# Performance work log

Hardware: AMD Instinct MI355X
Metric: run time of the kernel (lower is better)

Reference implementation:

```python
import jax, jax.numpy as jnp
import numpy as np

D = 1024
H = 16
HD = D // H
EPS = 1e-5

def _layernorm(x, g, b):
    mu = jnp.mean(x, axis=-1, keepdims=True)
    var = jnp.mean(jnp.square(x - mu), axis=-1, keepdims=True)
    return (x - mu) * jax.lax.rsqrt(var + EPS) * g + b

def setup_inputs() -> dict:
    key = jax.random.key(0)
    ks = jax.random.split(key, 12)
    B, Sq, Skv = 8, 1024, 1024
    s = 1.0 / np.sqrt(D)  # xavier-ish scale
    return {
        "Q": jax.random.normal(ks[0], (B, Sq, D), jnp.float32),
        "K": jax.random.normal(ks[1], (B, Skv, D), jnp.float32),
        "key_padding_mask": jnp.ones((B, Skv), jnp.int32),
        "Wq": jax.random.normal(ks[2], (D, D), jnp.float32) * s,
        "bq": jnp.zeros((D,), jnp.float32),
        "Wk": jax.random.normal(ks[3], (D, D), jnp.float32) * s,
        "bk": jnp.zeros((D,), jnp.float32),
        "Wv": jax.random.normal(ks[4], (D, D), jnp.float32) * s,
        "bv": jnp.zeros((D,), jnp.float32),
        "Wp": jax.random.normal(ks[5], (D, D), jnp.float32) * s,
        "bp": jnp.zeros((D,), jnp.float32),
        "g0": jnp.ones((D,), jnp.float32),
        "beta0": jnp.zeros((D,), jnp.float32),
        "g1": jnp.ones((D,), jnp.float32),
        "beta1": jnp.zeros((D,), jnp.float32),
    }

def reference(Q, K, key_padding_mask, Wq, bq, Wk, bk, Wv, bv, Wp, bp, g0, beta0, g1, beta1):
    B, Sq, _ = Q.shape
    q = Q @ Wq + bq                      # [B,Sq,D]
    k = K @ Wk + bk                      # [B,Skv,D]
    v = K @ Wv + bv
    qh = q.reshape(B, Sq, H, HD).transpose(0, 2, 1, 3)   # [B,H,Sq,hd]
    kh = k.reshape(B, -1, H, HD).transpose(0, 2, 1, 3)   # [B,H,Skv,hd]
    vh = v.reshape(B, -1, H, HD).transpose(0, 2, 1, 3)
    attn = jnp.einsum('bhqd,bhkd->bhqk', qh, kh) / np.sqrt(HD)
    pad = (key_padding_mask == 0)[:, None, None, :]      # [B,1,1,Skv]
    attn = jnp.where(pad, -jnp.inf, attn)
    attn = jax.nn.softmax(attn, axis=-1)
    ctx = jnp.einsum('bhqk,bhkd->bhqd', attn, vh)        # [B,H,Sq,hd]
    ctx = ctx.transpose(0, 2, 1, 3).reshape(B, Sq, H * HD)
    o = _layernorm(q + ctx, g0, beta0)
    o = _layernorm(o + jax.nn.gelu(o @ Wp + bp, approximate=False), g1, beta1)
    return o
```

## Files before the change

kernel.cpp:

```cpp
#include <hip/hip_runtime.h>
#include <hip/hip_bf16.h>
#include <math.h>

#define DEV __device__ __forceinline__

typedef __bf16 bf16;
typedef __bf16 bf16x8 __attribute__((ext_vector_type(8)));
typedef __bf16 bf16x4 __attribute__((ext_vector_type(4)));
typedef __bf16 bf16x2 __attribute__((ext_vector_type(2)));
typedef float f32x4 __attribute__((ext_vector_type(4)));
typedef float f32x16 __attribute__((ext_vector_type(16)));
typedef int i32x2 __attribute__((ext_vector_type(2)));
typedef unsigned int u32;
typedef unsigned long long u64;

static constexpr int BATCH = 8, S = 1024, D = 1024, H = 16, HD = 64;
static constexpr int M = BATCH * S;

static constexpr float QSCALE = 0.18033688f;
static constexpr float INVQSCALE = 5.54517744f;

DEV f32x4 mfma16(bf16x8 a, bf16x8 b, f32x4 c) {
  return __builtin_amdgcn_mfma_f32_16x16x32_bf16(a, b, c, 0, 0, 0);
}
DEV f32x16 mfma32(bf16x8 a, bf16x8 b, f32x16 c) {
  return __builtin_amdgcn_mfma_f32_32x32x16_bf16(a, b, c, 0, 0, 0);
}

DEV void gload_lds16(const void* g, void* l) {
  __builtin_amdgcn_global_load_lds(
      (__attribute__((address_space(1))) void*)(g),
      (__attribute__((address_space(3))) void*)(l), 16, 0, 0);
}

DEV bf16x8 lds_read8(const void* base, int byteoff) {
  return *(const bf16x8*)((const char*)base + byteoff);
}

DEV u32 packbf(float a, float b) {
  bf16x2 t = { (bf16)a, (bf16)b };
  return __builtin_bit_cast(u32, t);
}


__global__ void cvt_bf16_kernel(const float* __restrict__ in0, bf16* __restrict__ out0,
                                const float* __restrict__ in1, bf16* __restrict__ out1, int n) {
  const float* in = blockIdx.y ? in1 : in0;
  bf16* out = blockIdx.y ? out1 : out0;
  int i = (blockIdx.x * blockDim.x + threadIdx.x) * 4;
  int stride = gridDim.x * blockDim.x * 4;
  for (; i < n; i += stride) {
    float4 v = *(const float4*)(in + i);
    bf16x4 o = { (bf16)v.x, (bf16)v.y, (bf16)v.z, (bf16)v.w };
    *(bf16x4*)(out + i) = o;
  }
}

__global__ void transpose_cvt_kernel(const float* __restrict__ w0, bf16* __restrict__ o0,
                                     const float* __restrict__ w1, bf16* __restrict__ o1,
                                     const float* __restrict__ w2, bf16* __restrict__ o2,
                                     const float* __restrict__ w3, bf16* __restrict__ o3) {
  const int z = blockIdx.z;
  const float* in = z == 0 ? w0 : z == 1 ? w1 : z == 2 ? w2 : w3;
  bf16* out = z == 0 ? o0 : z == 1 ? o1 : z == 2 ? o2 : o3;
  __shared__ float t[32][33];
  int n0 = blockIdx.x * 32, k0 = blockIdx.y * 32;
  int tx = threadIdx.x, ty = threadIdx.y;
  for (int i = 0; i < 32; i += 8)
    t[ty + i][tx] = in[(size_t)(k0 + ty + i) * D + n0 + tx];
  __syncthreads();
  for (int i = 0; i < 32; i += 8)
    out[(size_t)(n0 + ty + i) * D + k0 + tx] = (bf16)t[tx][ty + i];
}


DEV void gemm_body(const bf16* A, const bf16* Bt, const float* bias,
                   bf16* Cb, float osc, bf16* As, bf16* Bs) {
  constexpr int K = 1024, N = 1024, BK = 32;
  const int tid = threadIdx.x, lane = tid & 63, wave = tid >> 6;
  const int lo = lane & 15, g = lane >> 4;
  int f = blockIdx.y * 8 + blockIdx.x;
  f = (f & 7) * 64 + (f >> 3);
  const int bm = f >> 3, bn = f & 7;
  const int wr = wave >> 1, wc = wave & 1;
  f32x4 acc[4][4] = {};
  const char* Ab = (const char*)(A + (size_t)bm * 128 * K);
  const char* Bb = (const char*)(Bt + (size_t)bn * 128 * K);

  const int srow[2] = { (wave * 2 + 0) * 16 + (lane >> 2), (wave * 2 + 1) * 16 + (lane >> 2) };
  const int sslot = lane & 3;

  for (int kt = 0; kt < K / BK; ++kt) {
    __syncthreads();
    const int k0b = kt * (BK * 2);
    for (int i = 0; i < 2; ++i) {
      int cbase = (wave * 2 + i) * 1024;
      int row = srow[i];
      int scol = ((sslot ^ (row & 3)) << 4);
      gload_lds16(Ab + (size_t)row * (K * 2) + k0b + scol, (char*)As + cbase);
      gload_lds16(Bb + (size_t)row * (K * 2) + k0b + scol, (char*)Bs + cbase);
    }
    __syncthreads();
    bf16x8 af[4], bfr[4];
    for (int mi = 0; mi < 4; ++mi) {
      int ar = wr * 64 + mi * 16 + lo;
      af[mi] = lds_read8(As, ar * 64 + ((g ^ (ar & 3)) << 4));
    }
    for (int ni = 0; ni < 4; ++ni) {
      int br = wc * 64 + ni * 16 + lo;
      bfr[ni] = lds_read8(Bs, br * 64 + ((g ^ (br & 3)) << 4));
    }
    for (int mi = 0; mi < 4; ++mi)
      for (int ni = 0; ni < 4; ++ni)
        acc[mi][ni] = mfma16(af[mi], bfr[ni], acc[mi][ni]);
  }

  const int rbase = bm * 128 + wr * 64;
  const int cbase = bn * 128 + wc * 64;
  for (int ni = 0; ni < 4; ++ni) {
    int col = cbase + ni * 16 + lo;
    float bv = bias[col];
    for (int mi = 0; mi < 4; ++mi) {
      int row0 = rbase + mi * 16 + g * 4;
      for (int r = 0; r < 4; ++r) {
        float v = acc[mi][ni][r] + bv;
        Cb[(size_t)(row0 + r) * N + col] = (bf16)(v * osc);
      }
    }
  }
}

__global__ __launch_bounds__(256) void gemm_qkv_kernel(
    const bf16* __restrict__ Qb, const bf16* __restrict__ Kb,
    const bf16* __restrict__ Wqt, const bf16* __restrict__ Wkt, const bf16* __restrict__ Wvt,
    const float* __restrict__ bq, const float* __restrict__ bk, const float* __restrict__ bv,
    bf16* __restrict__ qb, bf16* __restrict__ kb, bf16* __restrict__ vb)
{
  __shared__ bf16 As[128 * 32];
  __shared__ bf16 Bs[128 * 32];
  const int z = blockIdx.z;
  if (z == 0)      gemm_body(Qb, Wqt, bq, qb, QSCALE, As, Bs);
  else if (z == 1) gemm_body(Kb, Wkt, bk, kb, 1.f, As, Bs);
  else             gemm_body(Kb, Wvt, bv, vb, 1.f, As, Bs);
}

__global__ __launch_bounds__(256) void gemm_p_kernel(
    const bf16* __restrict__ A, const bf16* __restrict__ Bt,
    const float* __restrict__ bias, bf16* __restrict__ Cb)
{
  __shared__ bf16 As[128 * 32];
  __shared__ bf16 Bs[128 * 32];
  gemm_body(A, Bt, bias, Cb, 1.f, As, Bs);
}


DEV int swz(int row, int colb) { return row * 128 + (colb ^ ((row & 7) << 4)); }

__global__ __launch_bounds__(256, 3) void attn_kernel(
    const bf16* __restrict__ q, const bf16* __restrict__ k, const bf16* __restrict__ v,
    const int* __restrict__ mask, float* __restrict__ ctx)
{
  __shared__ bf16 Kl[2][64 * 64];
  __shared__ bf16 Vt[2][64 * 64];
  const int tid = threadIdx.x, lane = tid & 63, wave = tid >> 6;
  const int hi = lane >> 5, lq = lane & 31;
  const int wg = blockIdx.x;
  const int xcd = wg & 7, ix = wg >> 3;
  const int bh = xcd * 16 + (ix & 15);
  const int qt = ix >> 4;
  const int b = bh >> 4, h = bh & 15;
  const int q0 = qt * 128 + wave * 32;
  const size_t base = (size_t)b * S * D + (size_t)h * HD;

  bf16x8 qf[4];
#pragma unroll
  for (int hc = 0; hc < 4; ++hc)
    qf[hc] = *(const bf16x8*)(q + base + (size_t)(q0 + lq) * D + hc * 16 + hi * 8);

  f32x16 oaccT[2] = {};
  float mrow = -3e38f, lrow = 0.f;

  bf16x8 kst[2], vst[2];
  const int koff = tid * 16;
  const int krow = koff >> 7, kcol = koff & 127;

#define LOADK(KV0)                                                              \
  {                                                                             \
    _Pragma("unroll")                                                           \
    for (int rr = 0; rr < 2; ++rr)                                              \
      kst[rr] = *(const bf16x8*)((const char*)(k + base +                       \
                 (size_t)((KV0) + rr * 32 + krow) * D) + kcol);                 \
    _Pragma("unroll")                                                           \
    for (int rr = 0; rr < 2; ++rr) {                                            \
      int kvr = rr * 32 + wave * 8;                                             \
      _Pragma("unroll")                                                         \
      for (int i = 0; i < 8; ++i)                                               \
        vst[rr][i] = v[base + (size_t)((KV0) + kvr + i) * D + lane];            \
    }                                                                           \
  }

#define WRITEK(BI)                                                              \
  {                                                                             \
    _Pragma("unroll")                                                           \
    for (int rr = 0; rr < 2; ++rr)                                              \
      *(bf16x8*)((char*)Kl[BI] + swz(rr * 32 + krow, kcol)) = kst[rr];          \
    _Pragma("unroll")                                                           \
    for (int rr = 0; rr < 2; ++rr)                                              \
      *(bf16x8*)((char*)Vt[BI] + swz(lane, (rr * 32 + wave * 8) * 2)) = vst[rr];\
  }

  LOADK(0);
  WRITEK(0);

  for (int kt = 0; kt < S / 64; ++kt) {
    const int cur = kt & 1;
    const int kv0 = kt * 64;
    __syncthreads();
    if (kt < S / 64 - 1) LOADK(kv0 + 64);

    const char* Kb_ = (const char*)Kl[cur];
    const char* Vb_ = (const char*)Vt[cur];

    u64 mv = __ballot(mask[b * S + kv0 + lane] != 0);

    f32x16 sacc[2];
    __builtin_amdgcn_s_setprio(1);
#pragma unroll
    for (int sub = 0; sub < 2; ++sub) {
      f32x16 a = {};
#pragma unroll
      for (int hc = 0; hc < 4; ++hc) {
        bf16x8 kf = lds_read8(Kb_, swz(sub * 32 + lq, hc * 32 + hi * 16));
        a = mfma32(kf, qf[hc], a);
      }
      sacc[sub] = a;
    }
    __builtin_amdgcn_s_setprio(0);

    float mx = -3e38f;
    if (mv == ~0ull) {
#pragma unroll
      for (int sub = 0; sub < 2; ++sub)
#pragma unroll
        for (int r = 0; r < 16; ++r) mx = fmaxf(mx, sacc[sub][r]);
    } else {
      u64 mqh = mv >> (hi * 4);
#pragma unroll
      for (int sub = 0; sub < 2; ++sub)
#pragma unroll
        for (int rr = 0; rr < 4; ++rr)
#pragma unroll
          for (int rm = 0; rm < 4; ++rm) {
            int reg = rr * 4 + rm;
            bool ok = (mqh >> (rm + 8 * rr + 32 * sub)) & 1ull;
            float s = ok ? sacc[sub][reg] : -1e30f;
            sacc[sub][reg] = s;
            mx = fmaxf(mx, s);
          }
    }
    mx = fmaxf(mx, __shfl_xor(mx, 32));

    if (__any(mx > mrow + 11.5f)) {
      float mnew = fmaxf(mrow, mx);
      float fsc = exp2f(mrow - mnew);
      mrow = mnew;
      lrow *= fsc;
      oaccT[0] *= fsc;
      oaccT[1] *= fsc;
    }

    float rs = 0.f;
    u32 W[2][4][2];
#pragma unroll
    for (int sub = 0; sub < 2; ++sub)
#pragma unroll
      for (int rr = 0; rr < 4; ++rr)
#pragma unroll
        for (int hh = 0; hh < 2; ++hh) {
          float p0 = exp2f(sacc[sub][rr * 4 + 2 * hh] - mrow);
          float p1 = exp2f(sacc[sub][rr * 4 + 2 * hh + 1] - mrow);
          rs += p0 + p1;
          W[sub][rr][hh] = packbf(p0, p1);
        }
    rs += __shfl_xor(rs, 32);
    lrow += rs;

    bf16x8 pfr[4];
#pragma unroll
    for (int t = 0; t < 4; ++t) {
      const int sub = t >> 1, r0 = 2 * (t & 1);
      i32x2 s0 = __builtin_amdgcn_permlane32_swap(
          (int)W[sub][r0][0], (int)W[sub][r0 + 1][0], false, false);
      i32x2 s1 = __builtin_amdgcn_permlane32_swap(
          (int)W[sub][r0][1], (int)W[sub][r0 + 1][1], false, false);
      u32 wd[4] = { (u32)s0[0], (u32)s1[0], (u32)s0[1], (u32)s1[1] };
      pfr[t] = __builtin_bit_cast(bf16x8, wd);
    }

    __builtin_amdgcn_s_setprio(1);
#pragma unroll
    for (int hdsub = 0; hdsub < 2; ++hdsub) {
      f32x16 a = oaccT[hdsub];
#pragma unroll
      for (int t = 0; t < 4; ++t) {
        bf16x8 vf = lds_read8(Vb_, swz(hdsub * 32 + lq, t * 32 + hi * 16));
        a = mfma32(vf, pfr[t], a);
      }
      oaccT[hdsub] = a;
    }
    __builtin_amdgcn_s_setprio(0);

    if (kt < S / 64 - 1) WRITEK(cur ^ 1);
  }

  float linv = 1.0f / lrow;
  size_t rowb = ((size_t)b * S + q0 + lq) * D + (size_t)h * HD;
#pragma unroll
  for (int hdsub = 0; hdsub < 2; ++hdsub)
#pragma unroll
    for (int rr = 0; rr < 4; ++rr) {
      f32x4 o = { oaccT[hdsub][rr * 4 + 0] * linv, oaccT[hdsub][rr * 4 + 1] * linv,
                  oaccT[hdsub][rr * 4 + 2] * linv, oaccT[hdsub][rr * 4 + 3] * linv };
      *(f32x4*)(ctx + rowb + 32 * hdsub + 8 * rr + 4 * hi) = o;
    }
}


DEV void block_stats(float s, float s2, float* red, int tid, float& mu, float& rstd) {
  for (int off = 32; off > 0; off >>= 1) {
    s += __shfl_down(s, off);
    s2 += __shfl_down(s2, off);
  }
  int wave = tid >> 6, lane = tid & 63;
  if (lane == 0) { red[wave] = s; red[4 + wave] = s2; }
  __syncthreads();
  float S1 = red[0] + red[1] + red[2] + red[3];
  float S2 = red[4] + red[5] + red[6] + red[7];
  mu = S1 * (1.f / 1024.f);
  rstd = rsqrtf(S2 * (1.f / 1024.f) - mu * mu + 1e-5f);
}

__global__ __launch_bounds__(256) void ln0_kernel(
    const bf16* __restrict__ qb, const float* __restrict__ ctx,
    const float* __restrict__ g, const float* __restrict__ beta,
    bf16* __restrict__ ob)
{
  __shared__ float red[8];
  const int row = blockIdx.x, tid = threadIdx.x;
  const size_t base = (size_t)row * D;
  bf16x4 qv = *(const bf16x4*)(qb + base + tid * 4);
  float4 c = *(const float4*)(ctx + base + tid * 4);
  float x0 = (float)qv[0] * INVQSCALE + c.x;
  float x1 = (float)qv[1] * INVQSCALE + c.y;
  float x2 = (float)qv[2] * INVQSCALE + c.z;
  float x3 = (float)qv[3] * INVQSCALE + c.w;
  float mu, rstd;
  block_stats(x0 + x1 + x2 + x3,
              x0 * x0 + x1 * x1 + x2 * x2 + x3 * x3, red, tid, mu, rstd);
  float4 gv = *(const float4*)(g + tid * 4);
  float4 bv = *(const float4*)(beta + tid * 4);
  bf16x4 o = { (bf16)((x0 - mu) * rstd * gv.x + bv.x),
               (bf16)((x1 - mu) * rstd * gv.y + bv.y),
               (bf16)((x2 - mu) * rstd * gv.z + bv.z),
               (bf16)((x3 - mu) * rstd * gv.w + bv.w) };
  *(bf16x4*)(ob + base + tid * 4) = o;
}

DEV float gelu_exact(float t) { return 0.5f * t * (1.f + erff(t * 0.70710678118654752f)); }

__global__ __launch_bounds__(256) void ln1_kernel(
    const bf16* __restrict__ ob, const bf16* __restrict__ pb,
    const float* __restrict__ g, const float* __restrict__ beta,
    float* __restrict__ out)
{
  __shared__ float red[8];
  const int row = blockIdx.x, tid = threadIdx.x;
  const size_t base = (size_t)row * D;
  bf16x4 ov = *(const bf16x4*)(ob + base + tid * 4);
  bf16x4 pv = *(const bf16x4*)(pb + base + tid * 4);
  float x0 = (float)ov[0] + gelu_exact((float)pv[0]);
  float x1 = (float)ov[1] + gelu_exact((float)pv[1]);
  float x2 = (float)ov[2] + gelu_exact((float)pv[2]);
  float x3 = (float)ov[3] + gelu_exact((float)pv[3]);
  float mu, rstd;
  block_stats(x0 + x1 + x2 + x3,
              x0 * x0 + x1 * x1 + x2 * x2 + x3 * x3, red, tid, mu, rstd);
  float4 gv = *(const float4*)(g + tid * 4);
  float4 bv = *(const float4*)(beta + tid * 4);
  float o0 = (x0 - mu) * rstd * gv.x + bv.x;
  float o1 = (x1 - mu) * rstd * gv.y + bv.y;
  float o2 = (x2 - mu) * rstd * gv.z + bv.z;
  float o3 = (x3 - mu) * rstd * gv.w + bv.w;
  *(float4*)(out + base + tid * 4) = make_float4(o0, o1, o2, o3);
}


extern "C" void kernel_launch(void* const* d_in, const int* in_sizes, int n_in,
                              void* d_out, int out_size, void* d_ws, size_t ws_size,
                              hipStream_t stream) {
  const float* Q     = (const float*)d_in[0];
  const float* K     = (const float*)d_in[1];
  const int*   mask  = (const int*)d_in[2];
  const float* Wq    = (const float*)d_in[3];
  const float* bq    = (const float*)d_in[4];
  const float* Wk    = (const float*)d_in[5];
  const float* bk    = (const float*)d_in[6];
  const float* Wv    = (const float*)d_in[7];
  const float* bv    = (const float*)d_in[8];
  const float* Wp    = (const float*)d_in[9];
  const float* bp    = (const float*)d_in[10];
  const float* g0    = (const float*)d_in[11];
  const float* beta0 = (const float*)d_in[12];
  const float* g1    = (const float*)d_in[13];
  const float* beta1 = (const float*)d_in[14];
  float* out = (float*)d_out;

  char* w = (char*)d_ws;
  const size_t MB = 1u << 20;
  bf16* Qb  = (bf16*)(w + 0 * MB);
  bf16* Kb  = (bf16*)(w + 16 * MB);
  bf16* Wqt = (bf16*)(w + 32 * MB);
  bf16* Wkt = (bf16*)(w + 34 * MB);
  bf16* Wvt = (bf16*)(w + 36 * MB);
  bf16* Wpt = (bf16*)(w + 38 * MB);
  bf16* qb  = (bf16*)(w + 40 * MB);
  bf16* kb  = (bf16*)(w + 56 * MB);
  bf16* vb  = (bf16*)(w + 72 * MB);
  float* ctx = (float*)(w + 88 * MB);
  bf16* pb  = (bf16*)(w + 120 * MB);
  bf16* ob  = (bf16*)(w + 0 * MB);

  dim3 cg(1024, 2);
  cvt_bf16_kernel<<<cg, 256, 0, stream>>>(Q, Qb, K, Kb, M * D);
  dim3 tb(32, 8), tg(32, 32, 4);
  transpose_cvt_kernel<<<tg, tb, 0, stream>>>(Wq, Wqt, Wk, Wkt, Wv, Wvt, Wp, Wpt);

  dim3 gq(8, 64, 3);
  gemm_qkv_kernel<<<gq, 256, 0, stream>>>(Qb, Kb, Wqt, Wkt, Wvt, bq, bk, bv, qb, kb, vb);

  attn_kernel<<<1024, 256, 0, stream>>>(qb, kb, vb, mask, ctx);

  ln0_kernel<<<M, 256, 0, stream>>>(qb, ctx, g0, beta0, ob);
  dim3 gp(8, 64);
  gemm_p_kernel<<<gp, 256, 0, stream>>>(ob, Wpt, bp, pb);
  ln1_kernel<<<M, 256, 0, stream>>>(ob, pb, g1, beta1, out);
}
```

Baseline: 340.7 us.

## Emit V transposed from the QKV GEMM and load V^T tiles vectorized in attention

The V projection GEMM now swaps its MFMA operands so it writes V in a transposed [D, M] layout. The attention kernel can then load V tiles with 16-byte vector loads in the same pattern as K, replacing the 8 scalar strided bf16 loads per tile. The row-max and row-sum cross-half reductions also switch from __shfl_xor to permlane32_swap. The cost is that the transposed GEMM epilogue writes with a stride of M, which may coalesce less well.

```diff
diff --git a/kernel.cpp b/kernel.cpp
--- a/kernel.cpp
+++ b/kernel.cpp
@@ -40,6 +40,12 @@
 DEV u32 packbf(float a, float b) {
   bf16x2 t = { (bf16)a, (bf16)b };
   return __builtin_bit_cast(u32, t);
+}
+
+DEV float xor32_val(float x, int hi) {
+  int xi = __builtin_bit_cast(int, x);
+  i32x2 r = __builtin_amdgcn_permlane32_swap(xi, xi, false, false);
+  return __builtin_bit_cast(float, hi ? r[0] : r[1]);
 }
 
 
@@ -74,6 +80,7 @@
 }
 
 
+template<bool TRANS>
 DEV void gemm_body(const bf16* A, const bf16* Bt, const float* bias,
                    bf16* Cb, float osc, bf16* As, bf16* Bs) {
   constexpr int K = 1024, N = 1024, BK = 32;
@@ -111,22 +118,36 @@
       bfr[ni] = lds_read8(Bs, br * 64 + ((g ^ (br & 3)) << 4));
     }
     for (int mi = 0; mi < 4; ++mi)
-      for (int ni = 0; ni < 4; ++ni)
-        acc[mi][ni] = mfma16(af[mi], bfr[ni], acc[mi][ni]);
+      for (int ni = 0; ni < 4; ++ni) {
+        if (!TRANS) acc[mi][ni] = mfma16(af[mi], bfr[ni], acc[mi][ni]);
+        else        acc[ni][mi] = mfma16(bfr[ni], af[mi], acc[ni][mi]);
+      }
   }
 
   const int rbase = bm * 128 + wr * 64;
   const int cbase = bn * 128 + wc * 64;
-  for (int ni = 0; ni < 4; ++ni) {
-    int col = cbase + ni * 16 + lo;
-    float bv = bias[col];
-    for (int mi = 0; mi < 4; ++mi) {
-      int row0 = rbase + mi * 16 + g * 4;
+  if (!TRANS) {
+    for (int ni = 0; ni < 4; ++ni) {
+      int col = cbase + ni * 16 + lo;
+      float bv = bias[col];
+      for (int mi = 0; mi < 4; ++mi) {
+        int row0 = rbase + mi * 16 + g * 4;
+        for (int r = 0; r < 4; ++r) {
+          float v = acc[mi][ni][r] + bv;
+          Cb[(size_t)(row0 + r) * N + col] = (bf16)(v * osc);
+        }
+      }
+    }
+  } else {
+    for (int ni = 0; ni < 4; ++ni)
       for (int r = 0; r < 4; ++r) {
-        float v = acc[mi][ni][r] + bv;
-        Cb[(size_t)(row0 + r) * N + col] = (bf16)(v * osc);
+        int n = cbase + ni * 16 + g * 4 + r;
+        float bv = bias[n];
+        for (int mi = 0; mi < 4; ++mi) {
+          int m = rbase + mi * 16 + lo;
+          Cb[(size_t)n * M + m] = (bf16)(acc[ni][mi][r] + bv);
+        }
       }
-    }
   }
 }
 
@@ -134,14 +155,14 @@
     const bf16* __restrict__ Qb, const bf16* __restrict__ Kb,
     const bf16* __restrict__ Wqt, const bf16* __restrict__ Wkt, const bf16* __restrict__ Wvt,
     const float* __restrict__ bq, const float* __restrict__ bk, const float* __restrict__ bv,
-    bf16* __restrict__ qb, bf16* __restrict__ kb, bf16* __restrict__ vb)
+    bf16* __restrict__ qb, bf16* __restrict__ kb, bf16* __restrict__ vbt)
 {
   __shared__ bf16 As[128 * 32];
   __shared__ bf16 Bs[128 * 32];
   const int z = blockIdx.z;
-  if (z == 0)      gemm_body(Qb, Wqt, bq, qb, QSCALE, As, Bs);
-  else if (z == 1) gemm_body(Kb, Wkt, bk, kb, 1.f, As, Bs);
-  else             gemm_body(Kb, Wvt, bv, vb, 1.f, As, Bs);
+  if (z == 0)      gemm_body<false>(Qb, Wqt, bq, qb, QSCALE, As, Bs);
+  else if (z == 1) gemm_body<false>(Kb, Wkt, bk, kb, 1.f, As, Bs);
+  else             gemm_body<true >(Kb, Wvt, bv, vbt, 1.f, As, Bs);
 }
 
 __global__ __launch_bounds__(256) void gemm_p_kernel(
@@ -150,14 +171,14 @@
 {
   __shared__ bf16 As[128 * 32];
   __shared__ bf16 Bs[128 * 32];
-  gemm_body(A, Bt, bias, Cb, 1.f, As, Bs);
+  gemm_body<false>(A, Bt, bias, Cb, 1.f, As, Bs);
 }
 
 
 DEV int swz(int row, int colb) { return row * 128 + (colb ^ ((row & 7) << 4)); }
 
 __global__ __launch_bounds__(256, 3) void attn_kernel(
-    const bf16* __restrict__ q, const bf16* __restrict__ k, const bf16* __restrict__ v,
+    const bf16* __restrict__ q, const bf16* __restrict__ k, const bf16* __restrict__ vt,
     const int* __restrict__ mask, float* __restrict__ ctx)
 {
   __shared__ bf16 Kl[2][64 * 64];
@@ -183,40 +204,38 @@
   bf16x8 kst[2], vst[2];
   const int koff = tid * 16;
   const int krow = koff >> 7, kcol = koff & 127;
-
-#define LOADK(KV0)                                                              \
+  const bf16* vbase = vt + (size_t)(h * 64) * M + (size_t)b * S;
+
+#define LOADKV(KV0)                                                             \
   {                                                                             \
     _Pragma("unroll")                                                           \
     for (int rr = 0; rr < 2; ++rr)                                              \
       kst[rr] = *(const bf16x8*)((const char*)(k + base +                       \
                  (size_t)((KV0) + rr * 32 + krow) * D) + kcol);                 \
     _Pragma("unroll")                                                           \
-    for (int rr = 0; rr < 2; ++rr) {                                            \
-      int kvr = rr * 32 + wave * 8;                                             \
-      _Pragma("unroll")                                                         \
-      for (int i = 0; i < 8; ++i)                                               \
-        vst[rr][i] = v[base + (size_t)((KV0) + kvr + i) * D + lane];            \
-    }                                                                           \
-  }
-
-#define WRITEK(BI)                                                              \
+    for (int rr = 0; rr < 2; ++rr)                                              \
+      vst[rr] = *(const bf16x8*)((const char*)(vbase +                          \
+                 (size_t)(rr * 32 + krow) * M + (KV0)) + kcol);                 \
+  }
+
+#define WRITEKV(BI)                                                             \
   {                                                                             \
     _Pragma("unroll")                                                           \
     for (int rr = 0; rr < 2; ++rr)                                              \
       *(bf16x8*)((char*)Kl[BI] + swz(rr * 32 + krow, kcol)) = kst[rr];          \
     _Pragma("unroll")                                                           \
     for (int rr = 0; rr < 2; ++rr)                                              \
-      *(bf16x8*)((char*)Vt[BI] + swz(lane, (rr * 32 + wave * 8) * 2)) = vst[rr];\
-  }
-
-  LOADK(0);
-  WRITEK(0);
+      *(bf16x8*)((char*)Vt[BI] + swz(rr * 32 + krow, kcol)) = vst[rr];          \
+  }
+
+  LOADKV(0);
+  WRITEKV(0);
 
   for (int kt = 0; kt < S / 64; ++kt) {
     const int cur = kt & 1;
     const int kv0 = kt * 64;
     __syncthreads();
-    if (kt < S / 64 - 1) LOADK(kv0 + 64);
+    if (kt < S / 64 - 1) LOADKV(kv0 + 64);
 
     const char* Kb_ = (const char*)Kl[cur];
     const char* Vb_ = (const char*)Vt[cur];
@@ -258,7 +277,7 @@
             mx = fmaxf(mx, s);
           }
     }
-    mx = fmaxf(mx, __shfl_xor(mx, 32));
+    mx = fmaxf(mx, xor32_val(mx, hi));
 
     if (__any(mx > mrow + 11.5f)) {
       float mnew = fmaxf(mrow, mx);
@@ -282,7 +301,7 @@
           rs += p0 + p1;
           W[sub][rr][hh] = packbf(p0, p1);
         }
-    rs += __shfl_xor(rs, 32);
+    rs += xor32_val(rs, hi);
     lrow += rs;
 
     bf16x8 pfr[4];
@@ -310,7 +329,7 @@
     }
     __builtin_amdgcn_s_setprio(0);
 
-    if (kt < S / 64 - 1) WRITEK(cur ^ 1);
+    if (kt < S / 64 - 1) WRITEKV(cur ^ 1);
   }
 
   float linv = 1.0f / lrow;
@@ -425,7 +444,7 @@
   bf16* Wpt = (bf16*)(w + 38 * MB);
   bf16* qb  = (bf16*)(w + 40 * MB);
   bf16* kb  = (bf16*)(w + 56 * MB);
-  bf16* vb  = (bf16*)(w + 72 * MB);
+  bf16* vbt = (bf16*)(w + 72 * MB);
   float* ctx = (float*)(w + 88 * MB);
   bf16* pb  = (bf16*)(w + 120 * MB);
   bf16* ob  = (bf16*)(w + 0 * MB);
@@ -436,9 +455,9 @@
   transpose_cvt_kernel<<<tg, tb, 0, stream>>>(Wq, Wqt, Wk, Wkt, Wv, Wvt, Wp, Wpt);
 
   dim3 gq(8, 64, 3);
-  gemm_qkv_kernel<<<gq, 256, 0, stream>>>(Qb, Kb, Wqt, Wkt, Wvt, bq, bk, bv, qb, kb, vb);
-
-  attn_kernel<<<1024, 256, 0, stream>>>(qb, kb, vb, mask, ctx);
+  gemm_qkv_kernel<<<gq, 256, 0, stream>>>(Qb, Kb, Wqt, Wkt, Wvt, bq, bk, bv, qb, kb, vbt);
+
+  attn_kernel<<<1024, 256, 0, stream>>>(qb, kb, vbt, mask, ctx);
 
   ln0_kernel<<<M, 256, 0, stream>>>(qb, ctx, g0, beta0, ob);
   dim3 gp(8, 64);
```

After: 321.7 us. 1.06x faster.
